# Kernel tuning notes

Measured on AMD Instinct MI355X. Metric: run time of the kernel, lower is better.

Reference implementation:

```python
import jax, jax.numpy as jnp
import numpy as np

# Fixed problem geometry: B equal-sized graphs with contiguous node ids.
B, N, E, F_IN, H, C = 64, 1024, 655360, 128, 128, 10
K1 = int(np.ceil(0.8 * N))    # 820 nodes/graph kept by pool1
K2 = int(np.ceil(0.8 * K1))   # 656 nodes/graph kept by pool2


def setup_inputs() -> dict:
    key = jax.random.key(0)
    ks = jax.random.split(key, 12)
    x = jax.random.normal(ks[0], (B * N, F_IN), jnp.float32)
    # intra-graph random edges, E//B per graph
    e_per = E // B
    local = jax.random.randint(ks[1], (2, E), 0, N)
    off = jnp.repeat(jnp.arange(B, dtype=jnp.int32) * N, e_per)
    edge_index = (local + off[None, :]).astype(jnp.int32)
    batch = jnp.repeat(jnp.arange(B, dtype=jnp.int32), N)

    def lin(k, i, o):
        return jax.random.normal(k, (i, o), jnp.float32) / np.sqrt(i)

    return {
        "x": x, "edge_index": edge_index, "batch": batch,
        "Wl1": lin(ks[2], F_IN, H), "bl1": jnp.zeros((H,), jnp.float32), "Wr1": lin(ks[3], F_IN, H),
        "Wl2": lin(ks[4], H, H),    "bl2": jnp.zeros((H,), jnp.float32), "Wr2": lin(ks[5], H, H),
        "pw1": jax.random.normal(ks[6], (H,), jnp.float32) / np.sqrt(H),
        "pw2": jax.random.normal(ks[7], (H,), jnp.float32) / np.sqrt(H),
        "fW1": lin(ks[8], 2 * H, H), "fb1": jnp.zeros((H,), jnp.float32),
        "fW2": lin(ks[9], H, C),     "fb2": jnp.zeros((C,), jnp.float32),
    }


def _sage(x, src, dst, em, Wl, bl, Wr, n):
    # PyG SAGEConv (aggr='mean'): lin_l(mean_{j->i} x_j) + lin_r(x_i)
    msg = x[src] * em[:, None]                                   # [E, d]
    s = jax.ops.segment_sum(msg, dst, num_segments=n)            # [n, d]
    cnt = jax.ops.segment_sum(em, dst, num_segments=n)           # [n]
    mean = s / jnp.maximum(cnt, 1.0)[:, None]
    return mean @ Wl + bl + x @ Wr


def _topk_pool(x, src, dst, em, n_per, k, w):
    # PyG TopKPooling: score = tanh(x.w/||w||); keep top-k per graph; gate kept x by score.
    score = jnp.tanh(x @ w / jnp.linalg.norm(w))                 # [B*n_per]
    _, idx = jax.lax.top_k(score.reshape(B, n_per), k)           # [B, k]
    idx = jnp.sort(idx, axis=1)
    perm = (idx + (jnp.arange(B) * n_per)[:, None]).reshape(-1)  # global kept ids [B*k]
    nx = x[perm] * score[perm][:, None]
    # relabel edges; drop edges touching removed nodes via mask
    inv = jnp.full((B * n_per,), -1, jnp.int32).at[perm].set(jnp.arange(B * k, dtype=jnp.int32))
    ns, nd = inv[src], inv[dst]
    nm = em * (ns >= 0).astype(x.dtype) * (nd >= 0).astype(x.dtype)
    return nx, jnp.maximum(ns, 0), jnp.maximum(nd, 0), nm


def _readout(h, k):
    g = h.reshape(B, k, H)
    return jnp.concatenate([g.mean(axis=1), g.max(axis=1)], axis=1)  # [B, 2H]


def reference(x, edge_index, batch, Wl1, bl1, Wr1, Wl2, bl2, Wr2,
              pw1, pw2, fW1, fb1, fW2, fb2):
    src, dst = edge_index[0], edge_index[1]
    em = jnp.ones((E,), x.dtype)
    h = jax.nn.relu(_sage(x, src, dst, em, Wl1, bl1, Wr1, B * N))
    h, src, dst, em = _topk_pool(h, src, dst, em, N, K1, pw1)
    x1 = _readout(h, K1)
    h = jax.nn.relu(_sage(h, src, dst, em, Wl2, bl2, Wr2, B * K1))
    h, src, dst, em = _topk_pool(h, src, dst, em, K1, K2, pw2)
    x2 = _readout(h, K2)
    z = jax.nn.relu((x1 + x2) @ fW1 + fb1)
    # dropout is identity in eval mode
    return z @ fW2 + fb2
```

## Files before the change

### kernel.cpp

```cpp
#include <hip/hip_runtime.h>
#include <cstdint>
#include <cstddef>

namespace {

constexpr int kB    = 64;
constexpr int kN    = 1024;
constexpr int kE    = 655360;
constexpr int kEper = kE / kB;
constexpr int kH    = 128;
constexpr int kK1   = 820;
constexpr int kK2   = 656;
constexpr int kM1   = kB * kN;
constexpr int kM2   = kB * kK1;
constexpr int kM3   = kB * kK2;
constexpr int kRChunks = 16;

typedef __attribute__((ext_vector_type(8))) short bf16x8;
typedef __attribute__((ext_vector_type(4))) float f32x4;

__device__ inline ushort f2bf(float f) {
  uint u = __float_as_uint(f);
  return (ushort)((u + 0x7fffu + ((u >> 16) & 1u)) >> 16);
}
__device__ inline float bf2f(ushort s) { return __uint_as_float(((uint)s) << 16); }

__device__ inline int block_scan_1024(int v, int* wsum ) {
  const int lane = threadIdx.x & 63;
  const int w    = threadIdx.x >> 6;
#pragma unroll
  for (int off = 1; off < 64; off <<= 1) {
    const int n = __shfl_up(v, off);
    if (lane >= off) v += n;
  }
  if (lane == 63) wsum[w] = v;
  __syncthreads();
  if (w == 0) {
    int s = (lane < 16) ? wsum[lane] : 0;
#pragma unroll
    for (int off = 1; off < 16; off <<= 1) {
      const int n = __shfl_up(s, off);
      if (lane >= off) s += n;
    }
    if (lane < 16) wsum[lane] = s;
  }
  __syncthreads();
  if (w > 0) v += wsum[w - 1];
  return v;
}

__global__ __launch_bounds__(256)
void prep_kernel(const float* __restrict__ Wl1, const float* __restrict__ Wr1,
                 const float* __restrict__ Wl2, const float* __restrict__ Wr2,
                 const float* __restrict__ pw1, const float* __restrict__ pw2,
                 ushort* __restrict__ W1h, ushort* __restrict__ W1l,
                 ushort* __restrict__ W2h, ushort* __restrict__ W2l,
                 float* __restrict__ pwn1, float* __restrict__ pwn2) {
  const int tid = threadIdx.x;
  if (blockIdx.x == 256) {
    __shared__ float sq[256];
    const float* pw = (tid < 128) ? pw1 : pw2;
    const int j = tid & 127;
    const float v = pw[j];
    sq[tid] = v * v;
    __syncthreads();
    const int base = (tid < 128) ? 0 : 128;
    float sum = 0.0f;
    for (int k = 0; k < 128; ++k) sum += sq[base + k];
    float* o = (tid < 128) ? pwn1 : pwn2;
    o[j] = v / sqrtf(sum);
    return;
  }
  const bool l2 = blockIdx.x >= 128;
  const int idx = (blockIdx.x & 127) * 256 + tid;
  const int n = idx >> 8, k = idx & 255;
  const float* Wl = l2 ? Wl2 : Wl1;
  const float* Wr = l2 ? Wr2 : Wr1;
  const float w = (k < 128) ? Wl[k * kH + n] : Wr[(k - 128) * kH + n];
  const ushort h = f2bf(w);
  (l2 ? W2h : W1h)[n * 256 + k] = h;
  (l2 ? W2l : W1l)[n * 256 + k] = f2bf(w - bf2f(h));
}

__global__ __launch_bounds__(1024)
void csr_build(const int* __restrict__ src, const int* __restrict__ dst,
               int* __restrict__ coff, int* __restrict__ ccur,
               int* __restrict__ ent) {
  __shared__ int cnt[1024];
  __shared__ int wsum[16];
  const int g   = blockIdx.x;
  const int tid = threadIdx.x;
  const int ebase = g * kEper;
  cnt[tid] = 0;
  __syncthreads();
  for (int e = tid; e < kEper; e += 1024)
    atomicAdd(&cnt[dst[ebase + e] & (kN - 1)], 1);
  __syncthreads();
  const int dg   = cnt[tid];
  const int incl = block_scan_1024(dg, wsum);
  const int start = ebase + incl - dg;
  coff[g * kN + tid] = start;
  ccur[g * kN + tid] = start + dg;
  __syncthreads();
  cnt[tid] = start;
  __syncthreads();
  for (int e = tid; e < kEper; e += 1024) {
    const int d   = dst[ebase + e] & (kN - 1);
    const int pos = atomicAdd(&cnt[d], 1);
    ent[pos] = src[ebase + e] & (kN - 1);
  }
}

__global__ __launch_bounds__(1024, 8)
void gather1_lds(const float* __restrict__ feat, const int* __restrict__ ent,
                 const int* __restrict__ off, const int* __restrict__ cursor,
                 float* __restrict__ aggout) {
  __shared__ float cache[1024 * 16];
  const int xcd   = blockIdx.x & 7;
  const int local = blockIdx.x >> 3;
  const int graph = xcd * 8 + (local >> 3);
  const int chunk = local & 7;
  const int tid   = threadIdx.x;
  const int gbase = graph << 10;

#pragma unroll
  for (int ps = 0; ps < 4; ++ps) {
    const int row = ps * 256 + (tid >> 2);
    const int q   = (tid & 3) * 4;
    const float4 v = *(const float4*)(feat + (size_t)(gbase + row) * kH + chunk * 16 + q);
    *(float4*)&cache[row * 16 + q] = v;
  }
  __syncthreads();

  const int grp = tid >> 2;
  const int q4  = (tid & 3) * 4;

  for (int it = 0; it < 4; ++it) {
    const int lnode = it * 256 + grp;
    const int node  = gbase + lnode;
    const int o0 = off[node];
    const int o1 = cursor[node];
    const int deg = o1 - o0;
    float4 acc = make_float4(0.f, 0.f, 0.f, 0.f);
    int pf[4];
#pragma unroll
    for (int i = 0; i < 4; ++i) pf[i] = (o0 + i < o1) ? ent[o0 + i] : 0;
    for (int eb = 0; eb < deg; eb += 4) {
      int nx[4];
#pragma unroll
      for (int i = 0; i < 4; ++i) {
        const int idx = o0 + eb + 4 + i;
        nx[i] = (idx < o1) ? ent[idx] : 0;
      }
#pragma unroll
      for (int i = 0; i < 4; ++i) {
        const float m = (eb + i < deg) ? 1.0f : 0.0f;
        const float4 v = *(const float4*)&cache[pf[i] * 16 + q4];
        acc.x = fmaf(v.x, m, acc.x);
        acc.y = fmaf(v.y, m, acc.y);
        acc.z = fmaf(v.z, m, acc.z);
        acc.w = fmaf(v.w, m, acc.w);
      }
#pragma unroll
      for (int i = 0; i < 4; ++i) pf[i] = nx[i];
    }
    const float r = 1.0f / fmaxf((float)deg, 1.0f);
    const f32x4 res = {acc.x * r, acc.y * r, acc.z * r, acc.w * r};
    __builtin_nontemporal_store(res, (f32x4*)(aggout + (size_t)node * kH + chunk * 16 + q4));
  }
}

__global__ __launch_bounds__(1024, 8)
void gather2_lds(const float* __restrict__ feat, const int* __restrict__ ent,
                 const int* __restrict__ off, const int* __restrict__ cursor,
                 const int* __restrict__ perm, const float* __restrict__ gsg,
                 float* __restrict__ aggout) {
  __shared__ float cache[1024 * 16];
  __shared__ float gs[1024];
  const int xcd   = blockIdx.x & 7;
  const int local = blockIdx.x >> 3;
  const int graph = xcd * 8 + (local >> 3);
  const int chunk = local & 7;
  const int tid   = threadIdx.x;
  const int gbase = graph << 10;

#pragma unroll
  for (int ps = 0; ps < 4; ++ps) {
    const int row = ps * 256 + (tid >> 2);
    const int q   = (tid & 3) * 4;
    const float4 v = *(const float4*)(feat + (size_t)(gbase + row) * kH + chunk * 16 + q);
    *(float4*)&cache[row * 16 + q] = v;
  }
  gs[tid] = gsg[gbase + tid];
  __syncthreads();

  const int grp = tid >> 2;
  const int q4  = (tid & 3) * 4;

  for (int it = 0; it < 4; ++it) {
    const int lnode = it * 256 + grp;
    int o0 = 0, o1 = 0;
    if (lnode < kK1) {
      const int orig = perm[graph * kK1 + lnode];
      o0 = off[orig];
      o1 = cursor[orig];
    }
    const int deg = o1 - o0;
    float4 acc = make_float4(0.f, 0.f, 0.f, 0.f);
    int cnt = 0;
    int pf[4];
#pragma unroll
    for (int i = 0; i < 4; ++i) pf[i] = (o0 + i < o1) ? ent[o0 + i] : 0;
    for (int eb = 0; eb < deg; eb += 4) {
      int nx[4];
#pragma unroll
      for (int i = 0; i < 4; ++i) {
        const int idx = o0 + eb + 4 + i;
        nx[i] = (idx < o1) ? ent[idx] : 0;
      }
#pragma unroll
      for (int i = 0; i < 4; ++i) {
        const float raw  = gs[pf[i]];
        const bool  kept = (raw > 0.5f) && (eb + i < deg);
        const float s    = kept ? raw - 2.0f : 0.0f;
        cnt += kept ? 1 : 0;
        const float4 v = *(const float4*)&cache[pf[i] * 16 + q4];
        acc.x = fmaf(v.x, s, acc.x);
        acc.y = fmaf(v.y, s, acc.y);
        acc.z = fmaf(v.z, s, acc.z);
        acc.w = fmaf(v.w, s, acc.w);
      }
#pragma unroll
      for (int i = 0; i < 4; ++i) pf[i] = nx[i];
    }
    const float r = 1.0f / fmaxf((float)cnt, 1.0f);
    const f32x4 res = {acc.x * r, acc.y * r, acc.z * r, acc.w * r};
    if (lnode < kK1)
      __builtin_nontemporal_store(res,
          (f32x4*)(aggout + (size_t)(graph * kK1 + lnode) * kH + chunk * 16 + q4));
  }
}

__global__ __launch_bounds__(256)
void sage_gemm_mfma(const float* __restrict__ meanb, const float* __restrict__ xsrc,
                    const int* __restrict__ perm, const float* __restrict__ gsc,
                    const ushort* __restrict__ WTh, const ushort* __restrict__ WTl,
                    const float* __restrict__ bias, const float* __restrict__ pwn,
                    float* __restrict__ outp, float* __restrict__ scr) {
  __shared__ __align__(16) ushort aH[64][32];
  __shared__ __align__(16) ushort aL[64][32];
  __shared__ __align__(16) ushort wHs[128][32];
  __shared__ __align__(16) ushort wLs[128][32];
  __shared__ float sdot[64][2];
  const int tid  = threadIdx.x;
  const int wid  = tid >> 6;
  const int lane = tid & 63;
  const int quad = lane >> 4;
  const int l16  = lane & 15;
  const int rowbase = blockIdx.x * 64;
  const int wr = (wid >> 1) * 32;
  const int wc = (wid & 1) * 64;

  f32x4 acc[2][4];
#pragma unroll
  for (int a = 0; a < 2; ++a)
#pragma unroll
    for (int b = 0; b < 4; ++b) acc[a][b] = (f32x4){0.f, 0.f, 0.f, 0.f};

  for (int s = 0; s < 8; ++s) {
    const bool ismean = s < 4;
    const float* sp = ismean ? meanb : xsrc;
    const int kbase = s * 32;
    const int kloc  = ismean ? kbase : kbase - 128;
#pragma unroll
    for (int i = 0; i < 2; ++i) {
      const int p   = tid + i * 256;
      const int row = p >> 3;
      const int k4  = (p & 7) * 4;
      const int grow = rowbase + row;
      int srow = grow; float scale = 1.0f;
      if (perm) { if (!ismean) { srow = perm[grow]; scale = gsc[grow]; } }
      const float4 v = *(const float4*)(sp + (size_t)srow * kH + kloc + k4);
      float f[4] = {v.x * scale, v.y * scale, v.z * scale, v.w * scale};
      ushort4 hv, lv;
      hv.x = f2bf(f[0]); lv.x = f2bf(f[0] - bf2f(hv.x));
      hv.y = f2bf(f[1]); lv.y = f2bf(f[1] - bf2f(hv.y));
      hv.z = f2bf(f[2]); lv.z = f2bf(f[2] - bf2f(hv.z));
      hv.w = f2bf(f[3]); lv.w = f2bf(f[3] - bf2f(hv.w));
      *(ushort4*)&aH[row][k4] = hv;
      *(ushort4*)&aL[row][k4] = lv;
    }
#pragma unroll
    for (int i = 0; i < 4; ++i) {
      const int p  = tid + i * 256;
      const int n  = p >> 3;
      const int k4 = (p & 7) * 4;
      *(ushort4*)&wHs[n][k4] = *(const ushort4*)(WTh + n * 256 + kbase + k4);
      *(ushort4*)&wLs[n][k4] = *(const ushort4*)(WTl + n * 256 + kbase + k4);
    }
    __syncthreads();
    bf16x8 afh[2], afl[2];
#pragma unroll
    for (int rt = 0; rt < 2; ++rt) {
      afh[rt] = *(const bf16x8*)&aH[wr + rt * 16 + l16][quad * 8];
      afl[rt] = *(const bf16x8*)&aL[wr + rt * 16 + l16][quad * 8];
    }
#pragma unroll
    for (int ct = 0; ct < 4; ++ct) {
      const bf16x8 bh = *(const bf16x8*)&wHs[wc + ct * 16 + l16][quad * 8];
      const bf16x8 bl = *(const bf16x8*)&wLs[wc + ct * 16 + l16][quad * 8];
#pragma unroll
      for (int rt = 0; rt < 2; ++rt) {
        acc[rt][ct] = __builtin_amdgcn_mfma_f32_16x16x32_bf16(afh[rt], bh, acc[rt][ct], 0, 0, 0);
        acc[rt][ct] = __builtin_amdgcn_mfma_f32_16x16x32_bf16(afh[rt], bl, acc[rt][ct], 0, 0, 0);
        acc[rt][ct] = __builtin_amdgcn_mfma_f32_16x16x32_bf16(afl[rt], bh, acc[rt][ct], 0, 0, 0);
      }
    }
    __syncthreads();
  }
  float bv[4], pwv[4];
#pragma unroll
  for (int ct = 0; ct < 4; ++ct) {
    const int col = wc + ct * 16 + l16;
    bv[ct]  = bias[col];
    pwv[ct] = pwn[col];
  }
  float dot[2][4];
#pragma unroll
  for (int rt = 0; rt < 2; ++rt)
#pragma unroll
    for (int reg = 0; reg < 4; ++reg) dot[rt][reg] = 0.0f;
#pragma unroll
  for (int ct = 0; ct < 4; ++ct) {
    const int col = wc + ct * 16 + l16;
#pragma unroll
    for (int rt = 0; rt < 2; ++rt) {
#pragma unroll
      for (int reg = 0; reg < 4; ++reg) {
        const int row = rowbase + wr + rt * 16 + quad * 4 + reg;
        const float o = fmaxf(acc[rt][ct][reg] + bv[ct], 0.0f);
        outp[(size_t)row * kH + col] = o;
        dot[rt][reg] += o * pwv[ct];
      }
    }
  }
#pragma unroll
  for (int rt = 0; rt < 2; ++rt) {
#pragma unroll
    for (int reg = 0; reg < 4; ++reg) {
      float d = dot[rt][reg];
      d += __shfl_xor(d, 1);
      d += __shfl_xor(d, 2);
      d += __shfl_xor(d, 4);
      d += __shfl_xor(d, 8);
      if (l16 == 0) sdot[wr + rt * 16 + quad * 4 + reg][wc >> 6] = d;
    }
  }
  __syncthreads();
  if (tid < 64) scr[rowbase + tid] = tanhf(sdot[tid][0] + sdot[tid][1]);
}

__global__ __launch_bounds__(1024)
void rank_compact(const float* __restrict__ scr, int n_per, int K,
                  int* __restrict__ perm, float* __restrict__ gsc,
                  float* __restrict__ gsg) {
  __shared__ int hist[256];
  __shared__ int wsum[16];
  __shared__ uint bT;
  __shared__ int bRem;
  const int g = blockIdx.x, tid = threadIdx.x;
  const float sc = (tid < n_per) ? scr[g * n_per + tid] : -3e30f;
  const uint bits = __float_as_uint(sc);
  const uint key = (bits & 0x80000000u) ? ~bits : (bits | 0x80000000u);

  uint prefix = 0;
  int rem = K;
#pragma unroll
  for (int shift = 24; shift >= 0; shift -= 8) {
    if (tid < 256) hist[tid] = 0;
    __syncthreads();
    const uint mask = (shift == 24) ? 0u : (0xFFFFFFFFu << (shift + 8));
    if ((key & mask) == prefix)
      atomicAdd(&hist[(key >> shift) & 255], 1);
    __syncthreads();
    if (tid < 64) {
      const int h0 = hist[4 * tid + 0], h1 = hist[4 * tid + 1];
      const int h2 = hist[4 * tid + 2], h3 = hist[4 * tid + 3];
      const int loc = h0 + h1 + h2 + h3;
      int suf = loc;
#pragma unroll
      for (int d = 1; d < 64; d <<= 1) {
        const int o = __shfl_down(suf, d);
        if (tid + d < 64) suf += o;
      }
      const int above = suf - loc;
      int hs[5];
      hs[4] = above;
      hs[3] = above + h3;
      hs[2] = hs[3] + h2;
      hs[1] = hs[2] + h1;
      hs[0] = hs[1] + h0;
#pragma unroll
      for (int q = 0; q < 4; ++q) {
        if (hs[q] >= rem && hs[q + 1] < rem) {
          bT   = prefix | ((uint)(4 * tid + q) << shift);
          bRem = rem - hs[q + 1];
        }
      }
    }
    __syncthreads();
    prefix = bT;
    rem    = bRem;
  }
  const int gt = (key > prefix) ? 1 : 0;
  const int eq = (key == prefix) ? 1 : 0;
  const int incl = block_scan_1024((gt << 11) | eq, wsum);
  const int excl = incl - ((gt << 11) | eq);
  const int gt_excl = excl >> 11;
  const int eq_excl = excl & 2047;
  const int keep = (tid < n_per) && (gt || (eq && eq_excl < rem));
  if (keep) {
    const int pos = gt_excl + min(eq_excl, rem);
    perm[g * K + pos] = g * n_per + tid;
    gsc[g * K + pos]  = sc;
  }
  if (gsg) gsg[g * kN + tid] = keep ? sc + 2.0f : 0.0f;
}

__global__ __launch_bounds__(256)
void readout_part(const float* __restrict__ h, const int* __restrict__ perm,
                  const float* __restrict__ gsc, int K,
                  float* __restrict__ psum, float* __restrict__ pmax) {
  const int g     = blockIdx.x >> 4;
  const int chunk = blockIdx.x & (kRChunks - 1);
  const int j     = threadIdx.x & 127;
  const int part  = threadIdx.x >> 7;
  const int rows  = (K + kRChunks - 1) / kRChunks;
  const int r0 = chunk * rows;
  const int r1 = min(r0 + rows, K);
  float sum = 0.0f, mx = -1e30f;
  for (int r = r0 + part; r < r1; r += 2) {
    const int   row = perm[g * K + r];
    const float sc  = gsc[g * K + r];
    const float v   = h[(size_t)row * kH + j] * sc;
    sum += v;
    mx = fmaxf(mx, v);
  }
  __shared__ float ss[2][128], sm[2][128];
  ss[part][j] = sum;
  sm[part][j] = mx;
  __syncthreads();
  if (part == 0) {
    sum += ss[1][j];
    mx = fmaxf(mx, sm[1][j]);
    psum[(size_t)blockIdx.x * 128 + j] = sum;
    pmax[(size_t)blockIdx.x * 128 + j] = mx;
  }
}

__global__ __launch_bounds__(128)
void final_mlp(const float* __restrict__ ps1, const float* __restrict__ pm1,
               const float* __restrict__ ps2, const float* __restrict__ pm2,
               const float* __restrict__ fW1, const float* __restrict__ fb1,
               const float* __restrict__ fW2, const float* __restrict__ fb2,
               float* __restrict__ out) {
  __shared__ float xx[256];
  __shared__ float z[128];
  const int g = blockIdx.x, tid = threadIdx.x;
  float s1 = 0.f, m1 = -1e30f, s2 = 0.f, m2 = -1e30f;
#pragma unroll
  for (int c = 0; c < kRChunks; ++c) {
    s1 += ps1[(size_t)(g * kRChunks + c) * 128 + tid];
    m1 = fmaxf(m1, pm1[(size_t)(g * kRChunks + c) * 128 + tid]);
    s2 += ps2[(size_t)(g * kRChunks + c) * 128 + tid];
    m2 = fmaxf(m2, pm2[(size_t)(g * kRChunks + c) * 128 + tid]);
  }
  xx[tid]       = s1 / (float)kK1 + s2 / (float)kK2;
  xx[tid + 128] = m1 + m2;
  __syncthreads();
  float a = fb1[tid];
  for (int k = 0; k < 256; ++k) a += xx[k] * fW1[k * 128 + tid];
  z[tid] = fmaxf(a, 0.0f);
  __syncthreads();
  if (tid < 10) {
    float o = fb2[tid];
    for (int k = 0; k < 128; ++k) o += z[k] * fW2[k * 10 + tid];
    out[g * 10 + tid] = o;
  }
}

}

extern "C" void kernel_launch(void* const* d_in, const int* in_sizes, int n_in,
                              void* d_out, int out_size, void* d_ws, size_t ws_size,
                              hipStream_t stream) {
  const float* x   = (const float*)d_in[0];
  const int*   ei  = (const int*)d_in[1];
  const float* Wl1 = (const float*)d_in[3];
  const float* bl1 = (const float*)d_in[4];
  const float* Wr1 = (const float*)d_in[5];
  const float* Wl2 = (const float*)d_in[6];
  const float* bl2 = (const float*)d_in[7];
  const float* Wr2 = (const float*)d_in[8];
  const float* pw1 = (const float*)d_in[9];
  const float* pw2 = (const float*)d_in[10];
  const float* fW1 = (const float*)d_in[11];
  const float* fb1 = (const float*)d_in[12];
  const float* fW2 = (const float*)d_in[13];
  const float* fb2 = (const float*)d_in[14];
  const int* src = ei;
  const int* dst = ei + kE;
  (void)in_sizes; (void)n_in; (void)out_size; (void)ws_size;

  char* wsb = (char*)d_ws;
  size_t off_b = 0;
  auto alloc = [&](size_t bytes) {
    void* p = wsb + off_b;
    off_b += (bytes + 255) & ~(size_t)255;
    return p;
  };
  float* bufA = (float*)alloc((size_t)kM1 * kH * 4);
  float* bufB = (float*)alloc((size_t)kM1 * kH * 4);
  float* bufC = (float*)alloc((size_t)kM2 * kH * 4);
  int*   coff = (int*)alloc((size_t)kM1 * 4);
  int*   ccur = (int*)alloc((size_t)kM1 * 4);
  int*   ent  = (int*)alloc((size_t)kE * 4);
  float* scr  = (float*)alloc((size_t)kM1 * 4);
  float* gsg  = (float*)alloc((size_t)kM1 * 4);
  int*   perm1= (int*)alloc((size_t)kM2 * 4);
  float* gsc1 = (float*)alloc((size_t)kM2 * 4);
  int*   perm2= (int*)alloc((size_t)kM3 * 4);
  float* gsc2 = (float*)alloc((size_t)kM3 * 4);
  float* psum1= (float*)alloc((size_t)kB * kRChunks * 128 * 4);
  float* pmax1= (float*)alloc((size_t)kB * kRChunks * 128 * 4);
  float* psum2= (float*)alloc((size_t)kB * kRChunks * 128 * 4);
  float* pmax2= (float*)alloc((size_t)kB * kRChunks * 128 * 4);
  ushort* wt1h = (ushort*)alloc((size_t)128 * 256 * 2);
  ushort* wt1l = (ushort*)alloc((size_t)128 * 256 * 2);
  ushort* wt2h = (ushort*)alloc((size_t)128 * 256 * 2);
  ushort* wt2l = (ushort*)alloc((size_t)128 * 256 * 2);
  float* pwn1 = (float*)alloc(128 * 4);
  float* pwn2 = (float*)alloc(128 * 4);

  prep_kernel<<<257, 256, 0, stream>>>(Wl1, Wr1, Wl2, Wr2, pw1, pw2,
                                       wt1h, wt1l, wt2h, wt2l, pwn1, pwn2);

  csr_build<<<kB, 1024, 0, stream>>>(src, dst, coff, ccur, ent);
  gather1_lds<<<kB * 8, 1024, 0, stream>>>(x, ent, coff, ccur, bufA);
  sage_gemm_mfma<<<kM1 / 64, 256, 0, stream>>>(bufA, x, nullptr, nullptr,
                                               wt1h, wt1l, bl1, pwn1, bufB, scr);
  rank_compact<<<kB, 1024, 0, stream>>>(scr, kN, kK1, perm1, gsc1, gsg);
  readout_part<<<kB * kRChunks, 256, 0, stream>>>(bufB, perm1, gsc1, kK1, psum1, pmax1);

  gather2_lds<<<kB * 8, 1024, 0, stream>>>(bufB, ent, coff, ccur, perm1, gsg, bufA);
  sage_gemm_mfma<<<kM2 / 64, 256, 0, stream>>>(bufA, bufB, perm1, gsc1,
                                               wt2h, wt2l, bl2, pwn2, bufC, scr);
  rank_compact<<<kB, 1024, 0, stream>>>(scr, kK1, kK2, perm2, gsc2, nullptr);
  readout_part<<<kB * kRChunks, 256, 0, stream>>>(bufC, perm2, gsc2, kK2, psum2, pmax2);

  final_mlp<<<kB, 128, 0, stream>>>(psum1, pmax1, psum2, pmax2,
                                    fW1, fb1, fW2, fb2, (float*)d_out);
}
```

Baseline: 269.7 us.

## Fuse prep into CSR build and stream weights directly in SAGE GEMM

```diff
diff --git a/kernel.cpp b/kernel.cpp
--- a/kernel.cpp
+++ b/kernel.cpp
@@ -25,6 +25,21 @@
 }
 __device__ inline float bf2f(ushort s) { return __uint_as_float(((uint)s) << 16); }
 
+__device__ inline void cvt8(const float* f, uint* hh, uint* ll) {
+#pragma unroll
+  for (int i = 0; i < 4; ++i) {
+    uint h;
+    asm("v_cvt_pk_bf16_f32 %0, %1, %2" : "=v"(h) : "v"(f[2 * i]), "v"(f[2 * i + 1]));
+    const float r0 = __uint_as_float(h << 16);
+    const float r1 = __uint_as_float(h & 0xFFFF0000u);
+    const float d0 = f[2 * i] - r0;
+    const float d1 = f[2 * i + 1] - r1;
+    uint l;
+    asm("v_cvt_pk_bf16_f32 %0, %1, %2" : "=v"(l) : "v"(d0), "v"(d1));
+    hh[i] = h; ll[i] = l;
+  }
+}
+
 __device__ inline int block_scan_1024(int v, int* wsum ) {
   const int lane = threadIdx.x & 63;
   const int w    = threadIdx.x >> 6;
@@ -49,47 +64,44 @@
   return v;
 }
 
-__global__ __launch_bounds__(256)
-void prep_kernel(const float* __restrict__ Wl1, const float* __restrict__ Wr1,
-                 const float* __restrict__ Wl2, const float* __restrict__ Wr2,
-                 const float* __restrict__ pw1, const float* __restrict__ pw2,
-                 ushort* __restrict__ W1h, ushort* __restrict__ W1l,
-                 ushort* __restrict__ W2h, ushort* __restrict__ W2l,
-                 float* __restrict__ pwn1, float* __restrict__ pwn2) {
+__global__ __launch_bounds__(1024)
+void build_prep(const int* __restrict__ src, const int* __restrict__ dst,
+                int* __restrict__ coff, int* __restrict__ ccur,
+                int* __restrict__ ent,
+                const float* __restrict__ Wl1, const float* __restrict__ Wr1,
+                const float* __restrict__ Wl2, const float* __restrict__ Wr2,
+                const float* __restrict__ pw1, const float* __restrict__ pw2,
+                ushort* __restrict__ W1h, ushort* __restrict__ W1l,
+                ushort* __restrict__ W2h, ushort* __restrict__ W2l,
+                float* __restrict__ pwn1, float* __restrict__ pwn2) {
+  const int b   = blockIdx.x;
   const int tid = threadIdx.x;
-  if (blockIdx.x == 256) {
-    __shared__ float sq[256];
+  if (b >= 128) {
+    if (tid >= 256) return;
     const float* pw = (tid < 128) ? pw1 : pw2;
+    float* o        = (tid < 128) ? pwn1 : pwn2;
     const int j = tid & 127;
-    const float v = pw[j];
-    sq[tid] = v * v;
-    __syncthreads();
-    const int base = (tid < 128) ? 0 : 128;
     float sum = 0.0f;
-    for (int k = 0; k < 128; ++k) sum += sq[base + k];
-    float* o = (tid < 128) ? pwn1 : pwn2;
-    o[j] = v / sqrtf(sum);
+    for (int k = 0; k < 128; ++k) { const float v = pw[k]; sum += v * v; }
+    o[j] = pw[j] / sqrtf(sum);
     return;
   }
-  const bool l2 = blockIdx.x >= 128;
-  const int idx = (blockIdx.x & 127) * 256 + tid;
-  const int n = idx >> 8, k = idx & 255;
-  const float* Wl = l2 ? Wl2 : Wl1;
-  const float* Wr = l2 ? Wr2 : Wr1;
-  const float w = (k < 128) ? Wl[k * kH + n] : Wr[(k - 128) * kH + n];
-  const ushort h = f2bf(w);
-  (l2 ? W2h : W1h)[n * 256 + k] = h;
-  (l2 ? W2l : W1l)[n * 256 + k] = f2bf(w - bf2f(h));
-}
-
-__global__ __launch_bounds__(1024)
-void csr_build(const int* __restrict__ src, const int* __restrict__ dst,
-               int* __restrict__ coff, int* __restrict__ ccur,
-               int* __restrict__ ent) {
+  if (b >= 64) {
+    const int ob  = (b - 64) * 4 + (tid >> 8);
+    const bool l2 = ob >= 128;
+    const int idx = (ob & 127) * 256 + (tid & 255);
+    const int n = idx >> 8, k = idx & 255;
+    const float* Wl = l2 ? Wl2 : Wl1;
+    const float* Wr = l2 ? Wr2 : Wr1;
+    const float w = (k < 128) ? Wl[k * kH + n] : Wr[(k - 128) * kH + n];
+    const ushort h = f2bf(w);
+    (l2 ? W2h : W1h)[n * 256 + k] = h;
+    (l2 ? W2l : W1l)[n * 256 + k] = f2bf(w - bf2f(h));
+    return;
+  }
   __shared__ int cnt[1024];
   __shared__ int wsum[16];
-  const int g   = blockIdx.x;
-  const int tid = threadIdx.x;
+  const int g = b;
   const int ebase = g * kEper;
   cnt[tid] = 0;
   __syncthreads();
@@ -247,10 +259,8 @@
                     const ushort* __restrict__ WTh, const ushort* __restrict__ WTl,
                     const float* __restrict__ bias, const float* __restrict__ pwn,
                     float* __restrict__ outp, float* __restrict__ scr) {
-  __shared__ __align__(16) ushort aH[64][32];
-  __shared__ __align__(16) ushort aL[64][32];
-  __shared__ __align__(16) ushort wHs[128][32];
-  __shared__ __align__(16) ushort wLs[128][32];
+  __shared__ __align__(16) ushort aH[2][64][32];
+  __shared__ __align__(16) ushort aL[2][64][32];
   __shared__ float sdot[64][2];
   const int tid  = threadIdx.x;
   const int wid  = tid >> 6;
@@ -261,6 +271,14 @@
   const int wr = (wid >> 1) * 32;
   const int wc = (wid & 1) * 64;
 
+  const int arow = tid >> 2;
+  const int k8   = (tid & 3) * 8;
+  const int grow = rowbase + arow;
+  int prow = grow; float pscale = 1.0f;
+  if (perm) { prow = perm[grow]; pscale = gsc[grow]; }
+  const float* mrow = meanb + (size_t)grow * kH;
+  const float* xrow = xsrc + (size_t)prow * kH;
+
   f32x4 acc[2][4];
 #pragma unroll
   for (int a = 0; a < 2; ++a)
@@ -269,54 +287,41 @@
 
   for (int s = 0; s < 8; ++s) {
     const bool ismean = s < 4;
-    const float* sp = ismean ? meanb : xsrc;
-    const int kbase = s * 32;
-    const int kloc  = ismean ? kbase : kbase - 128;
-#pragma unroll
-    for (int i = 0; i < 2; ++i) {
-      const int p   = tid + i * 256;
-      const int row = p >> 3;
-      const int k4  = (p & 7) * 4;
-      const int grow = rowbase + row;
-      int srow = grow; float scale = 1.0f;
-      if (perm) { if (!ismean) { srow = perm[grow]; scale = gsc[grow]; } }
-      const float4 v = *(const float4*)(sp + (size_t)srow * kH + kloc + k4);
-      float f[4] = {v.x * scale, v.y * scale, v.z * scale, v.w * scale};
-      ushort4 hv, lv;
-      hv.x = f2bf(f[0]); lv.x = f2bf(f[0] - bf2f(hv.x));
-      hv.y = f2bf(f[1]); lv.y = f2bf(f[1] - bf2f(hv.y));
-      hv.z = f2bf(f[2]); lv.z = f2bf(f[2] - bf2f(hv.z));
-      hv.w = f2bf(f[3]); lv.w = f2bf(f[3] - bf2f(hv.w));
-      *(ushort4*)&aH[row][k4] = hv;
-      *(ushort4*)&aL[row][k4] = lv;
-    }
-#pragma unroll
-    for (int i = 0; i < 4; ++i) {
-      const int p  = tid + i * 256;
-      const int n  = p >> 3;
-      const int k4 = (p & 7) * 4;
-      *(ushort4*)&wHs[n][k4] = *(const ushort4*)(WTh + n * 256 + kbase + k4);
-      *(ushort4*)&wLs[n][k4] = *(const ushort4*)(WTl + n * 256 + kbase + k4);
-    }
+    const float* sp = ismean ? mrow : xrow;
+    const float sc  = ismean ? 1.0f : pscale;
+    const int kloc  = (ismean ? s : s - 4) * 32;
+    const float4 va = *(const float4*)(sp + kloc + k8);
+    const float4 vb = *(const float4*)(sp + kloc + k8 + 4);
+    float f[8] = {va.x * sc, va.y * sc, va.z * sc, va.w * sc,
+                  vb.x * sc, vb.y * sc, vb.z * sc, vb.w * sc};
+    uint hh[4], ll[4];
+    cvt8(f, hh, ll);
+    *(uint4*)&aH[s & 1][arow][k8] = make_uint4(hh[0], hh[1], hh[2], hh[3]);
+    *(uint4*)&aL[s & 1][arow][k8] = make_uint4(ll[0], ll[1], ll[2], ll[3]);
     __syncthreads();
     bf16x8 afh[2], afl[2];
 #pragma unroll
     for (int rt = 0; rt < 2; ++rt) {
-      afh[rt] = *(const bf16x8*)&aH[wr + rt * 16 + l16][quad * 8];
-      afl[rt] = *(const bf16x8*)&aL[wr + rt * 16 + l16][quad * 8];
-    }
+      afh[rt] = *(const bf16x8*)&aH[s & 1][wr + rt * 16 + l16][quad * 8];
+      afl[rt] = *(const bf16x8*)&aL[s & 1][wr + rt * 16 + l16][quad * 8];
+    }
+    const int kbase = s * 32;
+    bf16x8 bh[4], bl[4];
 #pragma unroll
     for (int ct = 0; ct < 4; ++ct) {
-      const bf16x8 bh = *(const bf16x8*)&wHs[wc + ct * 16 + l16][quad * 8];
-      const bf16x8 bl = *(const bf16x8*)&wLs[wc + ct * 16 + l16][quad * 8];
+      const size_t wo = (size_t)(wc + ct * 16 + l16) * 256 + kbase + quad * 8;
+      bh[ct] = *(const bf16x8*)(WTh + wo);
+      bl[ct] = *(const bf16x8*)(WTl + wo);
+    }
+#pragma unroll
+    for (int ct = 0; ct < 4; ++ct) {
 #pragma unroll
       for (int rt = 0; rt < 2; ++rt) {
-        acc[rt][ct] = __builtin_amdgcn_mfma_f32_16x16x32_bf16(afh[rt], bh, acc[rt][ct], 0, 0, 0);
-        acc[rt][ct] = __builtin_amdgcn_mfma_f32_16x16x32_bf16(afh[rt], bl, acc[rt][ct], 0, 0, 0);
-        acc[rt][ct] = __builtin_amdgcn_mfma_f32_16x16x32_bf16(afl[rt], bh, acc[rt][ct], 0, 0, 0);
-      }
-    }
-    __syncthreads();
+        acc[rt][ct] = __builtin_amdgcn_mfma_f32_16x16x32_bf16(afh[rt], bh[ct], acc[rt][ct], 0, 0, 0);
+        acc[rt][ct] = __builtin_amdgcn_mfma_f32_16x16x32_bf16(afh[rt], bl[ct], acc[rt][ct], 0, 0, 0);
+        acc[rt][ct] = __builtin_amdgcn_mfma_f32_16x16x32_bf16(afl[rt], bh[ct], acc[rt][ct], 0, 0, 0);
+      }
+    }
   }
   float bv[4], pwv[4];
 #pragma unroll
@@ -542,10 +547,10 @@
   float* pwn1 = (float*)alloc(128 * 4);
   float* pwn2 = (float*)alloc(128 * 4);
 
-  prep_kernel<<<257, 256, 0, stream>>>(Wl1, Wr1, Wl2, Wr2, pw1, pw2,
+  build_prep<<<129, 1024, 0, stream>>>(src, dst, coff, ccur, ent,
+                                       Wl1, Wr1, Wl2, Wr2, pw1, pw2,
                                        wt1h, wt1l, wt2h, wt2l, pwn1, pwn2);
 
-  csr_build<<<kB, 1024, 0, stream>>>(src, dst, coff, ccur, ent);
   gather1_lds<<<kB * 8, 1024, 0, stream>>>(x, ent, coff, ccur, bufA);
   sage_gemm_mfma<<<kM1 / 64, 256, 0, stream>>>(bufA, x, nullptr, nullptr,
                                                wt1h, wt1l, bl1, pwn1, bufB, scr);
```

New measurement: 291.6 us. +8.1%, slower.
